# Kernel tuning notes

Hardware: AMD Instinct MI355X
Metric: run time of the kernel (lower is better)

The kernel has to match this reference:

```python
import jax, jax.numpy as jnp
import numpy as np

EPS = 1e-7  # Keras K.epsilon()


def setup_inputs() -> dict:
    key = jax.random.key(0)
    k_x, k_w, k_b, k_u = jax.random.split(key, 4)
    B, T, D, A = 256, 512, 256, 50
    x = jax.random.normal(k_x, (B, T, D), dtype=jnp.float32)
    # Keras initializers.get('normal') -> stddev 0.05 RandomNormal
    W = jax.random.normal(k_w, (D, A), dtype=jnp.float32) * 0.05
    b = jax.random.normal(k_b, (A,), dtype=jnp.float32) * 0.05
    u = jax.random.normal(k_u, (A, 1), dtype=jnp.float32) * 0.05
    return {"x": x, "W": W, "b": b, "u": u}


def reference(x, W, b, u):
    # uit: [B, T, A]
    uit = jnp.tanh(jnp.einsum('btd,da->bta', x, W) + b)
    # ait: [B, T] raw scores -> exp-normalize (as in original, no max-subtract)
    ait = jnp.einsum('bta,a->bt', uit, u[:, 0])
    ait = jnp.exp(ait)
    ait = ait / (jnp.sum(ait, axis=1, keepdims=True) + EPS)
    # weighted pool over time: [B, D]
    return jnp.einsum('btd,bt->bd', x, ait)
```

## Files before the change

kernel.cpp:

```cpp
#include <hip/hip_runtime.h>
#include <math.h>

#define B_  256
#define T_  512
#define D_  256
#define A_  50
#define EPS 1e-7f
#define NW  16

typedef short  short8  __attribute__((ext_vector_type(8)));
typedef float  floatx4 __attribute__((ext_vector_type(4)));

__device__ inline unsigned short f2bf(float f) {
    unsigned int u = __float_as_uint(f);
    u = (u + 0x7fffu + ((u >> 16) & 1u)) >> 16;
    return (unsigned short)u;
}

__global__ void prep_kernel(const float* __restrict__ W,
                            const float* __restrict__ bias,
                            const float* __restrict__ u,
                            unsigned short* __restrict__ Wf,
                            float* __restrict__ bu64)
{
    int idx = blockIdx.x * 256 + threadIdx.x;
    int j  = idx & 7;
    int l  = (idx >> 3) & 63;
    int ks = (idx >> 9) & 7;
    int nt = idx >> 12;
    int n  = nt * 16 + (l & 15);
    int k  = ks * 32 + (l >> 4) * 8 + j;
    float val = (n < A_) ? W[k * A_ + n] : 0.0f;
    Wf[idx] = f2bf(val);
    if (idx < 64) {
        bu64[idx]      = (idx < A_) ? bias[idx] : 0.0f;
        bu64[64 + idx] = (idx < A_) ? u[idx]    : 0.0f;
    }
}

__global__ __launch_bounds__(1024)
void fused_kernel(const float* __restrict__ x,
                  const unsigned short* __restrict__ Wf,
                  const float* __restrict__ bu64,
                  float* __restrict__ out)
{
    __shared__ float s_lds[T_];
    __shared__ float part[NW * 256];

    const int tid  = threadIdx.x;
    const int w    = tid >> 6;
    const int l    = tid & 63;
    const int c    = l & 15;
    const int quad = l >> 4;
    const int bb   = blockIdx.x;

    const float*  __restrict__ xb  = x + (size_t)bb * T_ * D_;
    const short8* __restrict__ wf8 = (const short8*)Wf;

    float bnc[4], unc[4];
    #pragma unroll
    for (int nt = 0; nt < 4; nt++) {
        bnc[nt] = bu64[nt * 16 + c];
        unc[nt] = bu64[64 + nt * 16 + c];
    }

    #pragma unroll
    for (int pass = 0; pass < 2; pass++) {
        const int rowbase = pass * 256 + w * 16;
        const float4* __restrict__ xrow =
            (const float4*)(xb + (size_t)(rowbase + c) * D_);

        floatx4 acc[4];
        #pragma unroll
        for (int nt = 0; nt < 4; nt++) acc[nt] = (floatx4){0.f, 0.f, 0.f, 0.f};

        #pragma unroll
        for (int ks = 0; ks < 8; ks++) {
            const float4 a0 = xrow[ks * 8 + quad * 2];
            const float4 a1 = xrow[ks * 8 + quad * 2 + 1];
            short8 av;
            av[0] = (short)f2bf(a0.x); av[1] = (short)f2bf(a0.y);
            av[2] = (short)f2bf(a0.z); av[3] = (short)f2bf(a0.w);
            av[4] = (short)f2bf(a1.x); av[5] = (short)f2bf(a1.y);
            av[6] = (short)f2bf(a1.z); av[7] = (short)f2bf(a1.w);
            #pragma unroll
            for (int nt = 0; nt < 4; nt++) {
                const short8 bv = wf8[(nt * 8 + ks) * 64 + l];
                acc[nt] = __builtin_amdgcn_mfma_f32_16x16x32_bf16(av, bv, acc[nt], 0, 0, 0);
            }
        }

        #pragma unroll
        for (int r = 0; r < 4; r++) {
            float v = 0.0f;
            #pragma unroll
            for (int nt = 0; nt < 4; nt++)
                v += tanhf(acc[nt][r] + bnc[nt]) * unc[nt];
            #pragma unroll
            for (int off = 1; off < 16; off <<= 1)
                v += __shfl_xor(v, off, 16);
            if (c == 0)
                s_lds[rowbase + quad * 4 + r] = expf(v);
        }
    }
    __syncthreads();

    if (tid < 512) part[tid] = s_lds[tid];
    __syncthreads();
    for (int off = 256; off > 0; off >>= 1) {
        if (tid < off) part[tid] += part[tid + off];
        __syncthreads();
    }
    const float inv = 1.0f / (part[0] + EPS);
    __syncthreads();

    float4 acc2 = make_float4(0.f, 0.f, 0.f, 0.f);
    const int t0 = w * 32;
    #pragma unroll
    for (int i = 0; i < 32; i++) {
        const float4 xv = *(const float4*)(xb + (size_t)(t0 + i) * D_ + l * 4);
        const float sv  = s_lds[t0 + i];
        acc2.x += xv.x * sv;
        acc2.y += xv.y * sv;
        acc2.z += xv.z * sv;
        acc2.w += xv.w * sv;
    }
    acc2.x *= inv; acc2.y *= inv; acc2.z *= inv; acc2.w *= inv;

    part[w * 256 + l * 4 + 0] = acc2.x;
    part[w * 256 + l * 4 + 1] = acc2.y;
    part[w * 256 + l * 4 + 2] = acc2.z;
    part[w * 256 + l * 4 + 3] = acc2.w;
    __syncthreads();

    if (tid < 256) {
        float o = 0.0f;
        #pragma unroll
        for (int wv = 0; wv < NW; wv++) o += part[wv * 256 + tid];
        out[(size_t)bb * 256 + tid] = o;
    }
}

extern "C" void kernel_launch(void* const* d_in, const int* in_sizes, int n_in,
                              void* d_out, int out_size, void* d_ws, size_t ws_size,
                              hipStream_t stream)
{
    const float* x = (const float*)d_in[0];
    const float* W = (const float*)d_in[1];
    const float* b = (const float*)d_in[2];
    const float* u = (const float*)d_in[3];

    unsigned short* Wf  = (unsigned short*)d_ws;
    float*         bu64 = (float*)(Wf + 16384);
    float*         out  = (float*)d_out;

    prep_kernel  <<<64,  256,  0, stream>>>(W, b, u, Wf, bu64);
    fused_kernel <<<B_,  1024, 0, stream>>>(x, Wf, bu64, out);
}
```

Measured before the change: 219.2 us.

## Prefetch x rows into registers and use packed bf16 conversion intrinsics

```diff
diff --git a/kernel.cpp b/kernel.cpp
--- a/kernel.cpp
+++ b/kernel.cpp
@@ -1,4 +1,5 @@
 #include <hip/hip_runtime.h>
+#include <hip/hip_bf16.h>
 #include <math.h>
 
 #define B_  256
@@ -38,7 +39,21 @@
     }
 }
 
-__global__ __launch_bounds__(1024)
+__device__ inline void pack_bf4(short8& av, int base, float fx, float fy,
+                                float fz, float fw)
+{
+    union { __hip_bfloat162 h2; int i; } c0, c1;
+    c0.h2 = __float22bfloat162_rn(make_float2(fx, fy));
+    c1.h2 = __float22bfloat162_rn(make_float2(fz, fw));
+    union { int i[4]; short8 s8; } pk;
+    av[base + 0] = (short)(c0.i & 0xffff);
+    av[base + 1] = (short)((unsigned)c0.i >> 16);
+    av[base + 2] = (short)(c1.i & 0xffff);
+    av[base + 3] = (short)((unsigned)c1.i >> 16);
+    (void)pk;
+}
+
+__global__ __launch_bounds__(1024, 4)
 void fused_kernel(const float* __restrict__ x,
                   const unsigned short* __restrict__ Wf,
                   const float* __restrict__ bu64,
@@ -70,19 +85,22 @@
         const float4* __restrict__ xrow =
             (const float4*)(xb + (size_t)(rowbase + c) * D_);
 
+        float4 pre[16];
+        #pragma unroll
+        for (int i = 0; i < 16; i++)
+            pre[i] = xrow[(i >> 1) * 8 + quad * 2 + (i & 1)];
+
         floatx4 acc[4];
         #pragma unroll
         for (int nt = 0; nt < 4; nt++) acc[nt] = (floatx4){0.f, 0.f, 0.f, 0.f};
 
         #pragma unroll
         for (int ks = 0; ks < 8; ks++) {
-            const float4 a0 = xrow[ks * 8 + quad * 2];
-            const float4 a1 = xrow[ks * 8 + quad * 2 + 1];
+            const float4 a0 = pre[2 * ks];
+            const float4 a1 = pre[2 * ks + 1];
             short8 av;
-            av[0] = (short)f2bf(a0.x); av[1] = (short)f2bf(a0.y);
-            av[2] = (short)f2bf(a0.z); av[3] = (short)f2bf(a0.w);
-            av[4] = (short)f2bf(a1.x); av[5] = (short)f2bf(a1.y);
-            av[6] = (short)f2bf(a1.z); av[7] = (short)f2bf(a1.w);
+            pack_bf4(av, 0, a0.x, a0.y, a0.z, a0.w);
+            pack_bf4(av, 4, a1.x, a1.y, a1.z, a1.w);
             #pragma unroll
             for (int nt = 0; nt < 4; nt++) {
                 const short8 bv = wf8[(nt * 8 + ks) * 64 + l];
```

Result: no change. 220.6 us (+0.6%).
